# Performance work log

Measured on AMD Instinct MI355X. Metric: run time of the kernel, lower is better.

## Reference

```python
import jax, jax.numpy as jnp
import numpy as np

BS, N, FEAT = 4, 4096, 64
LN_EPS = 1e-5


def setup_inputs() -> dict:
    key = jax.random.key(0)
    k1, k2, k3 = jax.random.split(key, 3)
    positions = jax.random.normal(k1, (BS, N, 3), dtype=jnp.float32)
    # nn.Linear(n_point, feature_dim): weight (FEAT, N), bias (FEAT,)
    W = jax.random.normal(k2, (FEAT, N), dtype=jnp.float32) * (1.0 / np.sqrt(N))
    b = jax.random.normal(k3, (FEAT,), dtype=jnp.float32) * 0.02
    gamma = jnp.ones((FEAT,), dtype=jnp.float32)
    beta = jnp.zeros((FEAT,), dtype=jnp.float32)
    return {"positions": positions, "W": W, "b": b, "gamma": gamma, "beta": beta}


def reference(positions, W, b, gamma, beta):
    # all-pairs squared distances: (bs, N, N)
    diff = positions[:, :, None, :] - positions[:, None, :, :]  # (bs,N,N,3)
    sq = jnp.sum(diff * diff, axis=-1)                          # (bs,N,N)
    # safe sqrt (diagonal is exactly 0)
    safe = jnp.where(sq > 0, sq, 1.0)
    dist = jnp.where(sq > 0, jnp.sqrt(safe), 0.0)               # (bs,N,N)
    # Linear(N -> FEAT)
    x = jnp.einsum('bnm,fm->bnf', dist, W) + b                  # (bs,N,FEAT)
    # LayerNorm over last dim (biased variance, eps=1e-5)
    mu = jnp.mean(x, axis=-1, keepdims=True)
    var = jnp.mean((x - mu) ** 2, axis=-1, keepdims=True)
    xn = (x - mu) / jnp.sqrt(var + LN_EPS) * gamma + beta
    # SiLU
    return xn * jax.nn.sigmoid(xn)
```

## Files before the change

kernel.cpp:

```cpp
#include <hip/hip_runtime.h>


typedef float f32x4 __attribute__((ext_vector_type(4)));
typedef __bf16 bf16x8 __attribute__((ext_vector_type(8)));

union BF8 { bf16x8 v; uint4 u; };

#define N_PTS 4096
#define FEATD 64
#define BK 256
#define NCH (N_PTS / BK)

__global__ void wconv_kernel(const float* __restrict__ W,
                             unsigned short* __restrict__ Wbt) {
  int gid = blockIdx.x * blockDim.x + threadIdx.x;
  int f = gid >> 9, m8 = gid & 511;
  const float4* src = (const float4*)(W + (size_t)f * N_PTS + m8 * 8);
  float4 a = src[0], b = src[1];
  BF8 o;
  o.v[0] = (__bf16)a.x; o.v[1] = (__bf16)a.y; o.v[2] = (__bf16)a.z; o.v[3] = (__bf16)a.w;
  o.v[4] = (__bf16)b.x; o.v[5] = (__bf16)b.y; o.v[6] = (__bf16)b.z; o.v[7] = (__bf16)b.w;
  ((uint4*)Wbt)[(size_t)m8 * 64 + f] = o.u;
}

__device__ __forceinline__ void load_lds16(const void* g, void* l) {
  __builtin_amdgcn_global_load_lds(
      (const __attribute__((address_space(1))) void*)g,
      (__attribute__((address_space(3))) void*)l, 16, 0, 0);
}

__global__ __launch_bounds__(1024, 4) void frp_kernel(
    const float* __restrict__ pos, const float* __restrict__ W,
    const float* __restrict__ bias, const float* __restrict__ gamma,
    const float* __restrict__ beta, const unsigned short* __restrict__ Wbt,
    float* __restrict__ out) {
  __shared__ uint4 Wbuf[2][2048];
  __shared__ __align__(16) float Px[N_PTS];
  __shared__ __align__(16) float Py[N_PTS];
  __shared__ __align__(16) float Pz[N_PTS];

  const int tid = threadIdx.x;
  const int lane = tid & 63;
  const int wave = tid >> 6;
  const int rowgroup = wave & 3;
  const int khalf = wave >> 2;
  const int fx = lane & 15;
  const int q = lane >> 4;

  const int batch = blockIdx.x >> 6;
  const int nb = (blockIdx.x & 63) * 64;
  const float* posB = pos + (size_t)batch * N_PTS * 3;

  {
    const float4* p4 = (const float4*)posB;
    float4 f0 = p4[tid * 3 + 0];
    float4 f1 = p4[tid * 3 + 1];
    float4 f2 = p4[tid * 3 + 2];
    ((float4*)Px)[tid] = make_float4(f0.x, f0.w, f1.z, f2.y);
    ((float4*)Py)[tid] = make_float4(f0.y, f1.x, f1.w, f2.z);
    ((float4*)Pz)[tid] = make_float4(f0.z, f1.y, f2.x, f2.w);
  }

  const bool useWb = (Wbt != nullptr);

  auto stageW = [&](int c, int b) {
#pragma unroll
    for (int it = 0; it < 2; ++it) {
      int gi = it * 1024 + tid;
      if (useWb) {
        load_lds16(Wbt + ((size_t)c * 2048 + gi) * 8, &Wbuf[b][gi]);
      } else {
        int g = gi >> 6, f = gi & 63;
        const float4* src = (const float4*)(W + (size_t)f * N_PTS + c * BK + g * 8);
        float4 a = src[0], b2 = src[1];
        BF8 o;
        o.v[0] = (__bf16)a.x;  o.v[1] = (__bf16)a.y;  o.v[2] = (__bf16)a.z;  o.v[3] = (__bf16)a.w;
        o.v[4] = (__bf16)b2.x; o.v[5] = (__bf16)b2.y; o.v[6] = (__bf16)b2.z; o.v[7] = (__bf16)b2.w;
        Wbuf[b][gi] = o.u;
      }
    }
  };

  f32x4 acc[4];
#pragma unroll
  for (int t = 0; t < 4; ++t) acc[t] = (f32x4){0.f, 0.f, 0.f, 0.f};

  stageW(0, 0);
  __syncthreads();

  const int nrow = nb + rowgroup * 16 + fx;
  const float px = Px[nrow], py = Py[nrow], pz = Pz[nrow];

  for (int c = 0; c < NCH; ++c) {
    if (c + 1 < NCH) stageW(c + 1, (c + 1) & 1);
    const uint4* Wcur = Wbuf[c & 1];
#pragma unroll
    for (int ks = 0; ks < 2; ++ks) {
      const int g8 = khalf * 8 + ks * 4 + q;
      const int m4 = c * 64 + g8 * 2;
      f32x4 xa = ((const f32x4*)Px)[m4], xb = ((const f32x4*)Px)[m4 + 1];
      f32x4 ya = ((const f32x4*)Py)[m4], yb = ((const f32x4*)Py)[m4 + 1];
      f32x4 za = ((const f32x4*)Pz)[m4], zb = ((const f32x4*)Pz)[m4 + 1];
      f32x4 dxa = xa - px, dya = ya - py, dza = za - pz;
      f32x4 dxb = xb - px, dyb = yb - py, dzb = zb - pz;
      f32x4 sqa = dxa * dxa + dya * dya + dza * dza;
      f32x4 sqb = dxb * dxb + dyb * dyb + dzb * dzb;
      bf16x8 af;
#pragma unroll
      for (int j = 0; j < 4; ++j) af[j] = (__bf16)__builtin_amdgcn_sqrtf(sqa[j]);
#pragma unroll
      for (int j = 0; j < 4; ++j) af[4 + j] = (__bf16)__builtin_amdgcn_sqrtf(sqb[j]);
#pragma unroll
      for (int t = 0; t < 4; ++t) {
        BF8 bw;
        bw.u = Wcur[g8 * 64 + t * 16 + fx];
        acc[t] = __builtin_amdgcn_mfma_f32_16x16x32_bf16(af, bw.v, acc[t], 0, 0, 0);
      }
    }
    __syncthreads();
  }

  float* mb = (float*)Wbuf;
  const int lslot = rowgroup * 64 + lane;
  if (khalf > 0) {
#pragma unroll
    for (int t = 0; t < 4; ++t)
#pragma unroll
      for (int r = 0; r < 4; ++r)
        mb[(khalf - 1) * 4096 + (t * 4 + r) * 256 + lslot] = acc[t][r];
  }
  __syncthreads();
  if (khalf == 0) {
#pragma unroll
    for (int s = 0; s < 3; ++s)
#pragma unroll
      for (int t = 0; t < 4; ++t)
#pragma unroll
        for (int r = 0; r < 4; ++r)
          acc[t][r] += mb[s * 4096 + (t * 4 + r) * 256 + lslot];

    float bb[4], gg[4], be[4];
#pragma unroll
    for (int t = 0; t < 4; ++t) {
      bb[t] = bias[t * 16 + fx];
      gg[t] = gamma[t * 16 + fx];
      be[t] = beta[t * 16 + fx];
    }
    float* outB = out + ((size_t)batch * N_PTS + nb + rowgroup * 16) * FEATD;
#pragma unroll
    for (int r = 0; r < 4; ++r) {
      float x[4], d[4];
#pragma unroll
      for (int t = 0; t < 4; ++t) x[t] = acc[t][r] + bb[t];
      float s = x[0] + x[1] + x[2] + x[3];
      s += __shfl_xor(s, 1); s += __shfl_xor(s, 2);
      s += __shfl_xor(s, 4); s += __shfl_xor(s, 8);
      float mu = s * (1.f / 64.f);
      float v = 0.f;
#pragma unroll
      for (int t = 0; t < 4; ++t) { d[t] = x[t] - mu; v += d[t] * d[t]; }
      v += __shfl_xor(v, 1); v += __shfl_xor(v, 2);
      v += __shfl_xor(v, 4); v += __shfl_xor(v, 8);
      float rstd = __builtin_amdgcn_rsqf(v * (1.f / 64.f) + 1e-5f);
      float* orow = outB + (q * 4 + r) * FEATD;
#pragma unroll
      for (int t = 0; t < 4; ++t) {
        float xn = d[t] * rstd * gg[t] + be[t];
        float y = xn * (1.f / (1.f + __expf(-xn)));
        orow[t * 16 + fx] = y;
      }
    }
  }
}

extern "C" void kernel_launch(void* const* d_in, const int* in_sizes, int n_in,
                              void* d_out, int out_size, void* d_ws, size_t ws_size,
                              hipStream_t stream) {
  const float* pos   = (const float*)d_in[0];
  const float* W     = (const float*)d_in[1];
  const float* bias  = (const float*)d_in[2];
  const float* gamma = (const float*)d_in[3];
  const float* beta  = (const float*)d_in[4];
  float* out = (float*)d_out;

  const size_t wb_bytes = (size_t)FEATD * N_PTS * sizeof(unsigned short);
  int use_ws = (d_ws != nullptr && ws_size >= wb_bytes);
  unsigned short* Wbt = use_ws ? (unsigned short*)d_ws : nullptr;

  if (use_ws) {
    wconv_kernel<<<dim3((FEATD * N_PTS / 8) / 256), dim3(256), 0, stream>>>(W, Wbt);
  }
  frp_kernel<<<dim3(256), dim3(1024), 0, stream>>>(pos, W, bias, gamma, beta, Wbt, out);
}
```

Before: 88.38 us.

## Remap waves to two row tiles per wave with 8-way K split

Waves are reassigned from 4 row groups × 4 K-slices to 2 row supertiles (32 rows each) × 8 K-slices. Each wave now computes two 16-row distance fragments from one set of LDS position loads and reuses each loaded W fragment for two MFMAs. This halves the W LDS reads per MFMA and cuts position reloads. The cost is twice the accumulator registers and a two-stage cross-wave reduction of 8 partial sums through LDS with extra barriers.

Measured after the change: 87.06 us. No clear change (-1.5%).

```diff
diff --git a/kernel.cpp b/kernel.cpp
--- a/kernel.cpp
+++ b/kernel.cpp
@@ -42,8 +42,8 @@
   const int tid = threadIdx.x;
   const int lane = tid & 63;
   const int wave = tid >> 6;
-  const int rowgroup = wave & 3;
-  const int khalf = wave >> 2;
+  const int rs  = wave & 1;
+  const int ksl = wave >> 1;
   const int fx = lane & 15;
   const int q = lane >> 4;
 
@@ -81,63 +81,95 @@
     }
   };
 
-  f32x4 acc[4];
-#pragma unroll
-  for (int t = 0; t < 4; ++t) acc[t] = (f32x4){0.f, 0.f, 0.f, 0.f};
+  f32x4 acc[2][4];
+#pragma unroll
+  for (int a = 0; a < 2; ++a)
+#pragma unroll
+    for (int t = 0; t < 4; ++t) acc[a][t] = (f32x4){0.f, 0.f, 0.f, 0.f};
 
   stageW(0, 0);
   __syncthreads();
 
-  const int nrow = nb + rowgroup * 16 + fx;
-  const float px = Px[nrow], py = Py[nrow], pz = Pz[nrow];
+  const int nrow0 = nb + rs * 32 + fx;
+  const float px0 = Px[nrow0],      py0 = Py[nrow0],      pz0 = Pz[nrow0];
+  const float px1 = Px[nrow0 + 16], py1 = Py[nrow0 + 16], pz1 = Pz[nrow0 + 16];
+
+  const int g8 = ksl * 4 + q;
 
   for (int c = 0; c < NCH; ++c) {
     if (c + 1 < NCH) stageW(c + 1, (c + 1) & 1);
     const uint4* Wcur = Wbuf[c & 1];
-#pragma unroll
-    for (int ks = 0; ks < 2; ++ks) {
-      const int g8 = khalf * 8 + ks * 4 + q;
-      const int m4 = c * 64 + g8 * 2;
-      f32x4 xa = ((const f32x4*)Px)[m4], xb = ((const f32x4*)Px)[m4 + 1];
-      f32x4 ya = ((const f32x4*)Py)[m4], yb = ((const f32x4*)Py)[m4 + 1];
-      f32x4 za = ((const f32x4*)Pz)[m4], zb = ((const f32x4*)Pz)[m4 + 1];
-      f32x4 dxa = xa - px, dya = ya - py, dza = za - pz;
-      f32x4 dxb = xb - px, dyb = yb - py, dzb = zb - pz;
-      f32x4 sqa = dxa * dxa + dya * dya + dza * dza;
-      f32x4 sqb = dxb * dxb + dyb * dyb + dzb * dzb;
-      bf16x8 af;
-#pragma unroll
-      for (int j = 0; j < 4; ++j) af[j] = (__bf16)__builtin_amdgcn_sqrtf(sqa[j]);
-#pragma unroll
-      for (int j = 0; j < 4; ++j) af[4 + j] = (__bf16)__builtin_amdgcn_sqrtf(sqb[j]);
-#pragma unroll
-      for (int t = 0; t < 4; ++t) {
-        BF8 bw;
-        bw.u = Wcur[g8 * 64 + t * 16 + fx];
-        acc[t] = __builtin_amdgcn_mfma_f32_16x16x32_bf16(af, bw.v, acc[t], 0, 0, 0);
-      }
+    const int m4 = c * 64 + g8 * 2;
+    f32x4 xa = ((const f32x4*)Px)[m4], xb = ((const f32x4*)Px)[m4 + 1];
+    f32x4 ya = ((const f32x4*)Py)[m4], yb = ((const f32x4*)Py)[m4 + 1];
+    f32x4 za = ((const f32x4*)Pz)[m4], zb = ((const f32x4*)Pz)[m4 + 1];
+
+    bf16x8 af0, af1;
+    {
+      f32x4 dx = xa - px0, dy = ya - py0, dz = za - pz0;
+      f32x4 sq = dx * dx + dy * dy + dz * dz;
+#pragma unroll
+      for (int j = 0; j < 4; ++j) af0[j] = (__bf16)__builtin_amdgcn_sqrtf(sq[j]);
+      dx = xb - px0; dy = yb - py0; dz = zb - pz0;
+      sq = dx * dx + dy * dy + dz * dz;
+#pragma unroll
+      for (int j = 0; j < 4; ++j) af0[4 + j] = (__bf16)__builtin_amdgcn_sqrtf(sq[j]);
+      dx = xa - px1; dy = ya - py1; dz = za - pz1;
+      sq = dx * dx + dy * dy + dz * dz;
+#pragma unroll
+      for (int j = 0; j < 4; ++j) af1[j] = (__bf16)__builtin_amdgcn_sqrtf(sq[j]);
+      dx = xb - px1; dy = yb - py1; dz = zb - pz1;
+      sq = dx * dx + dy * dy + dz * dz;
+#pragma unroll
+      for (int j = 0; j < 4; ++j) af1[4 + j] = (__bf16)__builtin_amdgcn_sqrtf(sq[j]);
+    }
+#pragma unroll
+    for (int t = 0; t < 4; ++t) {
+      BF8 bw;
+      bw.u = Wcur[g8 * 64 + t * 16 + fx];
+      acc[0][t] = __builtin_amdgcn_mfma_f32_16x16x32_bf16(af0, bw.v, acc[0][t], 0, 0, 0);
+      acc[1][t] = __builtin_amdgcn_mfma_f32_16x16x32_bf16(af1, bw.v, acc[1][t], 0, 0, 0);
     }
     __syncthreads();
   }
 
-  float* mb = (float*)Wbuf;
-  const int lslot = rowgroup * 64 + lane;
-  if (khalf > 0) {
-#pragma unroll
-    for (int t = 0; t < 4; ++t)
-#pragma unroll
-      for (int r = 0; r < 4; ++r)
-        mb[(khalf - 1) * 4096 + (t * 4 + r) * 256 + lslot] = acc[t][r];
-  }
-  __syncthreads();
-  if (khalf == 0) {
+  f32x4* mbv = (f32x4*)Wbuf;
+  __syncthreads();
+  if (ksl >= 4) {
+    int w = (ksl - 4) * 2 + rs;
+#pragma unroll
+    for (int a = 0; a < 2; ++a)
+#pragma unroll
+      for (int t = 0; t < 4; ++t)
+        mbv[w * 512 + (a * 4 + t) * 64 + lane] = acc[a][t];
+  }
+  __syncthreads();
+  if (ksl < 4) {
+    int w = ksl * 2 + rs;
+#pragma unroll
+    for (int a = 0; a < 2; ++a)
+#pragma unroll
+      for (int t = 0; t < 4; ++t)
+        acc[a][t] += mbv[w * 512 + (a * 4 + t) * 64 + lane];
+  }
+  __syncthreads();
+  if (ksl >= 1 && ksl < 4) {
+    int w = (ksl - 1) * 2 + rs;
+#pragma unroll
+    for (int a = 0; a < 2; ++a)
+#pragma unroll
+      for (int t = 0; t < 4; ++t)
+        mbv[w * 512 + (a * 4 + t) * 64 + lane] = acc[a][t];
+  }
+  __syncthreads();
+  if (ksl == 0) {
 #pragma unroll
     for (int s = 0; s < 3; ++s)
 #pragma unroll
-      for (int t = 0; t < 4; ++t)
-#pragma unroll
-        for (int r = 0; r < 4; ++r)
-          acc[t][r] += mb[s * 4096 + (t * 4 + r) * 256 + lslot];
+      for (int a = 0; a < 2; ++a)
+#pragma unroll
+        for (int t = 0; t < 4; ++t)
+          acc[a][t] += mbv[(s * 2 + rs) * 512 + (a * 4 + t) * 64 + lane];
 
     float bb[4], gg[4], be[4];
 #pragma unroll
@@ -146,28 +178,31 @@
       gg[t] = gamma[t * 16 + fx];
       be[t] = beta[t * 16 + fx];
     }
-    float* outB = out + ((size_t)batch * N_PTS + nb + rowgroup * 16) * FEATD;
-#pragma unroll
-    for (int r = 0; r < 4; ++r) {
-      float x[4], d[4];
-#pragma unroll
-      for (int t = 0; t < 4; ++t) x[t] = acc[t][r] + bb[t];
-      float s = x[0] + x[1] + x[2] + x[3];
-      s += __shfl_xor(s, 1); s += __shfl_xor(s, 2);
-      s += __shfl_xor(s, 4); s += __shfl_xor(s, 8);
-      float mu = s * (1.f / 64.f);
-      float v = 0.f;
-#pragma unroll
-      for (int t = 0; t < 4; ++t) { d[t] = x[t] - mu; v += d[t] * d[t]; }
-      v += __shfl_xor(v, 1); v += __shfl_xor(v, 2);
-      v += __shfl_xor(v, 4); v += __shfl_xor(v, 8);
-      float rstd = __builtin_amdgcn_rsqf(v * (1.f / 64.f) + 1e-5f);
-      float* orow = outB + (q * 4 + r) * FEATD;
-#pragma unroll
-      for (int t = 0; t < 4; ++t) {
-        float xn = d[t] * rstd * gg[t] + be[t];
-        float y = xn * (1.f / (1.f + __expf(-xn)));
-        orow[t * 16 + fx] = y;
+    float* outB = out + ((size_t)batch * N_PTS + nb + rs * 32) * FEATD;
+#pragma unroll
+    for (int a = 0; a < 2; ++a) {
+#pragma unroll
+      for (int r = 0; r < 4; ++r) {
+        float x[4], d[4];
+#pragma unroll
+        for (int t = 0; t < 4; ++t) x[t] = acc[a][t][r] + bb[t];
+        float s = x[0] + x[1] + x[2] + x[3];
+        s += __shfl_xor(s, 1); s += __shfl_xor(s, 2);
+        s += __shfl_xor(s, 4); s += __shfl_xor(s, 8);
+        float mu = s * (1.f / 64.f);
+        float v = 0.f;
+#pragma unroll
+        for (int t = 0; t < 4; ++t) { d[t] = x[t] - mu; v += d[t] * d[t]; }
+        v += __shfl_xor(v, 1); v += __shfl_xor(v, 2);
+        v += __shfl_xor(v, 4); v += __shfl_xor(v, 8);
+        float rstd = __builtin_amdgcn_rsqf(v * (1.f / 64.f) + 1e-5f);
+        float* orow = outB + (a * 16 + q * 4 + r) * FEATD;
+#pragma unroll
+        for (int t = 0; t < 4; ++t) {
+          float xn = d[t] * rstd * gg[t] + be[t];
+          float y = xn * (1.f / (1.f + __expf(-xn)));
+          orow[t * 16 + fx] = y;
+        }
       }
     }
   }
```
